# Kernel optimization log

Measured on AMD Instinct MI355X. Metric: run time of the kernel, lower is better.

## Reference

```python
import jax, jax.numpy as jnp
import numpy as np

S, V = 16, 8                 # node embedding irreps: 16x0e + 8x1o
GEO = 3 * V                  # flattened vector feature dims
OUT = 8                      # output irreps: 8x0e
RADIUS = 5.0
NUM_BASIS = 20               # radius * basis_density_per_A
ACT_NORM = 1.6789717         # e3nn normalize2mom constant for silu under N(0,1)
SQ3 = 3.0 ** 0.5
W_MSG = S*S + V*S + S*V + V*V        # 576 = weight_numel of node x sh -> node TP
W_REC = (S*S + V*V) * OUT            # 2560 = weight_numel of node x node -> 8x0e TP


def _mlp(x, w0, w1):
    # e3nn FullyConnectedNet: randn weights, matmul scaled by 1/sqrt(fan_in),
    # hidden activation is second-moment-normalized silu, last layer linear.
    h = jax.nn.silu(x @ (w0 / np.sqrt(w0.shape[0]))) * ACT_NORM
    return h @ (w1 / np.sqrt(w1.shape[0]))


def _sh(vec):
    # o3.spherical_harmonics lmax=1, normalize=True, normalization='component':
    # Y0 = 1, Y1 = sqrt(3) * unit_vector
    r = vec / jnp.linalg.norm(vec, axis=-1, keepdims=True)
    return jnp.ones((vec.shape[0], 1), vec.dtype), SQ3 * r


def _split(f):
    return f[:, :S], f[:, S:].reshape(-1, V, 3)


def _tp_node_sh(xf, y0, y1, w):
    # FullyConnectedTensorProduct (Sx0e+Vx1o) x (1x0e+1x1o) -> (Sx0e+Vx1o), external per-edge weights.
    # CG (e3nn wigner_3j): 0x0->0: 1; 1x1->0: delta/sqrt3; 0x1->1,1x0->1: delta/sqrt3.
    # path_weight = sqrt((2l_out+1)/fan_in), fan_in per output irrep = S*1 + V*1.
    xs, xv = _split(xf)
    o = 0
    wA = w[:, o:o + S*S].reshape(-1, S, S); o += S*S   # 0e x 0e -> 0e
    wB = w[:, o:o + V*S].reshape(-1, V, S); o += V*S   # 1o x 1o -> 0e
    wC = w[:, o:o + S*V].reshape(-1, S, V); o += S*V   # 0e x 1o -> 1o
    wD = w[:, o:].reshape(-1, V, V)                    # 1o x 0e -> 1o
    fan = float(S + V)
    pw0 = (1.0 / fan) ** 0.5
    pw1 = (3.0 / fan) ** 0.5
    out_s = pw0 * (jnp.einsum('eu,euw->ew', xs * y0, wA)
                   + jnp.einsum('eui,ei,euw->ew', xv, y1, wB) / SQ3)
    out_v = (pw1 / SQ3) * (jnp.einsum('eu,ei,euw->ewi', xs, y1, wC)
                           + jnp.einsum('eui,euw->ewi', xv * y0[..., None], wD))
    return jnp.concatenate([out_s, out_v.reshape(-1, GEO)], axis=1)


def _tp_rec(xf, yf, w):
    # FullyConnectedTensorProduct (node) x (node) -> OUTx0e, external per-edge weights.
    xs, xv = _split(xf)
    ys, yv = _split(yf)
    w1 = w[:, :S*S*OUT].reshape(-1, S, S, OUT)
    w2 = w[:, S*S*OUT:].reshape(-1, V, V, OUT)
    pw = (1.0 / float(S*S + V*V)) ** 0.5
    return pw * (jnp.einsum('eu,ev,euvw->ew', xs, ys, w1)
                 + jnp.einsum('eui,evi,euvw->ew', xv, yv, w2) / SQ3)


def _dist_embed(d):
    # soft_one_hot_linspace(basis='smooth_finite', cutoff=True) * sqrt(num_basis)
    values = jnp.linspace(0.0, RADIUS, NUM_BASIS + 2)[1:-1]
    step = RADIUS / (NUM_BASIS + 1)
    diff = (d[:, None] - values) / step
    sus = lambda t: jnp.where(t > 0.0, jnp.exp(-1.0 / jnp.where(t > 0.0, t, 1.0)), 0.0)
    return 1.14136 * np.exp(2.0) * sus(diff + 1.0) * sus(1.0 - diff) * (NUM_BASIS ** 0.5)


def _mp_step(node, pos, src, dst, edge_attr, imp, mw0, mw1, uw0, uw1, is_initial):
    n = node.shape[0]
    vec = pos[dst] - pos[src]
    y0, y1 = _sh(vec)
    tp = _tp_node_sh(node[src], y0, y1, _mlp(edge_attr, mw0, mw1))
    deg = src.shape[0] / n
    msgs = jax.ops.segment_sum(tp, dst, num_segments=n) / (deg ** 0.5)
    msgs = msgs * imp
    scal = _mlp(jnp.concatenate([msgs[:, :S], node[:, :S]], axis=1), uw0, uw1)
    geo = msgs[:, S:] + node[:, S:]
    if not is_initial:
        geo = geo * 0.5
    return jnp.concatenate([scal, geo], axis=1)


def _forward(x, pos, edge_attr, emb_w0, emb_w1, imp0, msg0_w0, msg0_w1, upd0_w0, upd0_w1,
             imp1, msg1_w0, msg1_w1, upd1_w0, upd1_w1, lig_w0, lig_w1, rec_w0, rec_w1,
             edge_index, inter_edge_index):
    src, dst = edge_index[0], edge_index[1]
    node = _mlp(x, emb_w0, emb_w1)                                   # [N, S]
    node = jnp.concatenate([node, jnp.zeros((node.shape[0], GEO), node.dtype)], axis=1)
    node = _mp_step(node, pos, src, dst, edge_attr, imp0, msg0_w0, msg0_w1, upd0_w0, upd0_w1, True)
    node = _mp_step(node, pos, src, dst, edge_attr, imp1, msg1_w0, msg1_w1, upd1_w0, upd1_w1, False)
    rec, lig = inter_edge_index[0], inter_edge_index[1]
    vec = pos[lig] - pos[rec]
    y0, y1 = _sh(vec)
    demb = _dist_embed(jnp.linalg.norm(vec, axis=1))
    lig_emb = _tp_node_sh(node[lig], y0, y1, _mlp(demb, lig_w0, lig_w1))
    return _tp_rec(lig_emb, node[rec], _mlp(demb, rec_w0, rec_w1))    # [E_inter, OUT]


def setup_inputs():
    key = jax.random.key(0)
    ks = iter(jax.random.split(key, 32))
    N, E, EI = 10000, 120000, 40000
    A, B = 10, 5   # len(atom_types), len(bond_types)
    rn = lambda *s: jax.random.normal(next(ks), s, dtype=jnp.float32)
    # edges without self-loops (dst != src) to keep edge_vec nonzero
    src = jax.random.randint(next(ks), (E,), 0, N)
    dst = (src + jax.random.randint(next(ks), (E,), 1, N)) % N
    irec = jax.random.randint(next(ks), (EI,), 0, N)
    ilig = (irec + jax.random.randint(next(ks), (EI,), 1, N)) % N
    return dict(
        x=jax.random.uniform(next(ks), (N, A), dtype=jnp.float32),
        pos=rn(N, 3) * 3.0,
        edge_index=jnp.stack([src, dst]),
        edge_attr=jax.random.uniform(next(ks), (E, B), dtype=jnp.float32),
        inter_edge_index=jnp.stack([irec, ilig]),
        emb_w0=rn(A, 64), emb_w1=rn(64, S),
        imp0=rn(1), msg0_w0=rn(B, 64), msg0_w1=rn(64, W_MSG),
        upd0_w0=rn(2 * S, 64), upd0_w1=rn(64, S),
        imp1=rn(1), msg1_w0=rn(B, 64), msg1_w1=rn(64, W_MSG),
        upd1_w0=rn(2 * S, 64), upd1_w1=rn(64, S),
        lig_w0=rn(NUM_BASIS, 64), lig_w1=rn(64, W_MSG),
        rec_w0=rn(NUM_BASIS, 64), rec_w1=rn(64, W_REC),
    )


def reference(x, pos, edge_index, edge_attr, inter_edge_index,
              emb_w0, emb_w1, imp0, msg0_w0, msg0_w1, upd0_w0, upd0_w1,
              imp1, msg1_w0, msg1_w1, upd1_w0, upd1_w1,
              lig_w0, lig_w1, rec_w0, rec_w1):
    return _forward(x, pos, edge_attr, emb_w0, emb_w1, imp0, msg0_w0, msg0_w1, upd0_w0, upd0_w1,
                    imp1, msg1_w0, msg1_w1, upd1_w0, upd1_w1, lig_w0, lig_w1, rec_w0, rec_w1,
                    edge_index, inter_edge_index)
```

## Files before the change

### kernel.cpp

```cpp
#include <hip/hip_runtime.h>
#include <hip/hip_fp16.h>
#include <cmath>

constexpr float ACT_NORM = 1.6789717f;
constexpr float PW0      = 0.20412414523193154f;
constexpr float PW1      = 0.35355339059327373f;
constexpr float PWREC    = 0.05590169943749474f;
constexpr float INV_SQ3  = 0.57735026918962576f;
constexpr float PW0s     = PW0 * 0.125f;
constexpr float PW1s     = PW1 * 0.125f;
constexpr float PWRECs   = PWREC * 0.125f;

__device__ __forceinline__ float silu_n(float x) {
  return x / (1.f + __expf(-x)) * ACT_NORM;
}

__device__ __forceinline__ unsigned ubcast_lane(unsigned v, int k) {
  return (unsigned)__builtin_amdgcn_readlane((int)v, k);
}

typedef _Float16 h2v __attribute__((ext_vector_type(2)));
typedef _Float16 f16x8 __attribute__((ext_vector_type(8)));
typedef float    f32x4 __attribute__((ext_vector_type(4)));

__device__ __forceinline__ unsigned packh2(float a, float b) {
  h2v p; p.x = (_Float16)a; p.y = (_Float16)b;
  return __builtin_bit_cast(unsigned, p);
}
__device__ __forceinline__ unsigned short f16bits(float a) {
  return __builtin_bit_cast(unsigned short, (_Float16)a);
}
__device__ __forceinline__ float h2f(unsigned short b) {
  return (float)__builtin_bit_cast(_Float16, b);
}
__device__ __forceinline__ float dot2h(unsigned w2, unsigned h2, float acc) {
  return __builtin_amdgcn_fdot2(__builtin_bit_cast(h2v, w2),
                                __builtin_bit_cast(h2v, h2), acc, false);
}
__device__ __forceinline__ float hlo(unsigned d) {
  return (float)__builtin_bit_cast(_Float16, (unsigned short)(d & 0xffffu));
}
__device__ __forceinline__ float hhi(unsigned d) {
  return (float)__builtin_bit_cast(_Float16, (unsigned short)(d >> 16));
}
__device__ __forceinline__ float hsel(unsigned d, int hi) { return hi ? hhi(d) : hlo(d); }
__device__ __forceinline__ unsigned u4sel(const uint4& v, int i) {
  return i == 0 ? v.x : (i == 1 ? v.y : (i == 2 ? v.z : v.w));
}
__device__ __forceinline__ unsigned u2sel(const uint2& v, int i) { return i ? v.y : v.x; }

__device__ __forceinline__ f32x4 mfma16(uint4 a, uint4 b, f32x4 c) {
  return __builtin_amdgcn_mfma_f32_16x16x32_f16(
      __builtin_bit_cast(f16x8, a), __builtin_bit_cast(f16x8, b), c, 0, 0, 0);
}

__global__ __launch_bounds__(256)
void hist_kernel(const int* __restrict__ ei, int* __restrict__ cnt, int E) {
  const int e = blockIdx.x * 256 + threadIdx.x;
  if (e < E) atomicAdd(&cnt[ei[E + e]], 1);
}

__global__ __launch_bounds__(1024)
void scan_kernel(const int* __restrict__ cnt, int* __restrict__ starts, int N) {
  __shared__ int sums[1024];
  const int t = threadIdx.x;
  const int per = (N + 1023) >> 10;
  const int base = t * per;
  int s = 0;
  for (int i = 0; i < per; ++i) {
    const int idx = base + i;
    if (idx < N) s += cnt[idx];
  }
  sums[t] = s;
  __syncthreads();
  for (int off = 1; off < 1024; off <<= 1) {
    int v = (t >= off) ? sums[t - off] : 0;
    __syncthreads();
    sums[t] += v;
    __syncthreads();
  }
  int run = (t > 0) ? sums[t - 1] : 0;
  for (int i = 0; i < per; ++i) {
    const int idx = base + i;
    if (idx < N) { starts[idx] = run; run += cnt[idx]; }
  }
}

__global__ __launch_bounds__(256)
void scatter_kernel(const int* __restrict__ ei, const int* __restrict__ starts,
                    int* __restrict__ cursor, int* __restrict__ eperm, int E) {
  const int e = blockIdx.x * 256 + threadIdx.x;
  if (e < E) {
    const int d = ei[E + e];
    const int r = atomicAdd(&cursor[d], 1);
    eperm[starts[d] + r] = e;
  }
}

__global__ __launch_bounds__(256)
void emb_kernel(const float* __restrict__ x, const float* __restrict__ w0,
                const float* __restrict__ w1, float* __restrict__ node, int N) {
  const int lane = threadIdx.x & 63;
  const int lw   = threadIdx.x >> 6;
  const int gw   = blockIdx.x * 4 + lw;
  __shared__ float sH[4][64];
  const bool valid = gw < N;
  const int n = valid ? gw : 0;
  float acc = 0.f;
#pragma unroll
  for (int a = 0; a < 10; ++a) acc = fmaf(x[n * 10 + a], w0[a * 64 + lane], acc);
  acc *= 0.31622776601683794f;
  sH[lw][lane] = silu_n(acc);
  __syncthreads();
  if (valid) {
    if (lane < 16) {
      float o = 0.f;
#pragma unroll
      for (int k = 0; k < 64; ++k) o = fmaf(sH[lw][k], w1[k * 16 + lane], o);
      node[(size_t)n * 40 + lane] = o * 0.125f;
    } else if (lane < 40) {
      node[(size_t)n * 40 + lane] = 0.f;
    }
  }
}

template <bool HALFMB>
__global__ __launch_bounds__(256)
void upd_kernel(float* __restrict__ node, const void* __restrict__ mbufv,
                const int* __restrict__ starts, const int* __restrict__ cnt,
                const int* __restrict__ eperm,
                const float* __restrict__ w0, const float* __restrict__ w1,
                const float* __restrict__ imp, float geo_scale, float inv_sqrt_deg, int N) {
  const int lane = threadIdx.x & 63;
  const int lw   = threadIdx.x >> 6;
  const int gw   = blockIdx.x * 4 + lw;
  __shared__ float sIn[4][32];
  __shared__ float sH[4][64];
  const bool valid = gw < N;
  const int n = valid ? gw : 0;
  const float mscale = imp[0] * inv_sqrt_deg;

  float m = 0.f;
  if (lane < 40) {
    const int s0 = starts[n], d = cnt[n];
    if (HALFMB) {
      const unsigned short* mb = (const unsigned short*)mbufv;
      for (int j = 0; j < d; ++j)
        m += h2f(mb[(size_t)eperm[s0 + j] * 40 + lane]);
    } else {
      const float* mb = (const float*)mbufv;
      for (int j = 0; j < d; ++j)
        m += mb[(size_t)eperm[s0 + j] * 40 + lane];
    }
  }

  if (lane < 16)      sIn[lw][lane] = m * mscale;
  else if (lane < 32) sIn[lw][lane] = node[(size_t)n * 40 + lane - 16];
  __syncthreads();
  float acc = 0.f;
#pragma unroll
  for (int a = 0; a < 32; ++a) acc = fmaf(sIn[lw][a], w0[a * 64 + lane], acc);
  acc *= 0.17677669529663687f;
  sH[lw][lane] = silu_n(acc);
  __syncthreads();
  if (valid) {
    if (lane < 16) {
      float o = 0.f;
#pragma unroll
      for (int k = 0; k < 64; ++k) o = fmaf(sH[lw][k], w1[k * 16 + lane], o);
      node[(size_t)n * 40 + lane] = o * 0.125f;
    } else if (lane < 40) {
      const size_t gi = (size_t)n * 40 + lane;
      node[gi] = fmaf(m, mscale, node[gi]) * geo_scale;
    }
  }
}

__global__ __launch_bounds__(256)
void inter_h_kernel(const float* __restrict__ pos, const int* __restrict__ iei,
                    const float* __restrict__ lw0, const float* __restrict__ rw0,
                    float* __restrict__ hL, float* __restrict__ hR, int EI) {
  const int lane = threadIdx.x & 63;
  const int lw   = threadIdx.x >> 6;
  const int gw   = blockIdx.x * 4 + lw;
  __shared__ float sD[4][20];
  const bool valid = gw < EI;
  const int e = valid ? gw : 0;
  const int rec = iei[e], lig = iei[EI + e];
  const float dx = pos[lig * 3]     - pos[rec * 3];
  const float dy = pos[lig * 3 + 1] - pos[rec * 3 + 1];
  const float dz = pos[lig * 3 + 2] - pos[rec * 3 + 2];
  const float d = sqrtf(dx * dx + dy * dy + dz * dz);
  if (lane < 20) {
    const float diff = d * 4.2f - (float)(lane + 1);
    const float t1 = diff + 1.f, t2 = 1.f - diff;
    float v = 0.f;
    if (t1 > 0.f && t2 > 0.f) {
      const float C = 1.14136f * 7.3890560989306495f * 4.4721359549995794f;
      v = C * __expf(-1.f / t1 - 1.f / t2);
    }
    sD[lw][lane] = v;
  }
  __syncthreads();
  float a0 = 0.f, a1 = 0.f;
#pragma unroll
  for (int b = 0; b < 20; ++b) {
    const float db = sD[lw][b];
    a0 = fmaf(db, lw0[b * 64 + lane], a0);
    a1 = fmaf(db, rw0[b * 64 + lane], a1);
  }
  a0 *= 0.22360679774997896f;
  a1 *= 0.22360679774997896f;
  if (valid) {
    hL[(size_t)e * 64 + lane] = silu_n(a0);
    hR[(size_t)e * 64 + lane] = silu_n(a1);
  }
}

__global__ __launch_bounds__(256)
void edge_hf_kernel(const float* __restrict__ eattr, const float* __restrict__ w0,
                    uint4* __restrict__ hEf, int E, int nTe) {
  const int gid = blockIdx.x * 256 + threadIdx.x;
  if (gid >= nTe * 128) return;
  const int T = gid >> 7, rem = gid & 127, H = rem >> 6, l = rem & 63;
  int e = T * 16 + (l & 15);
  if (e >= E) e = E - 1;
  const int k0 = H * 32 + (l >> 4) * 8;
  float ea[5];
#pragma unroll
  for (int a = 0; a < 5; ++a) ea[a] = eattr[(size_t)e * 5 + a] * 0.4472135954999579f;
  unsigned q[4];
#pragma unroll
  for (int jj = 0; jj < 4; ++jj) {
    float hh[2];
#pragma unroll
    for (int p = 0; p < 2; ++p) {
      const int k = k0 + jj * 2 + p;
      float acc = 0.f;
#pragma unroll
      for (int a = 0; a < 5; ++a) acc = fmaf(ea[a], w0[a * 64 + k], acc);
      hh[p] = silu_n(acc);
    }
    q[jj] = packh2(hh[0], hh[1]);
  }
  uint4 out; out.x = q[0]; out.y = q[1]; out.z = q[2]; out.w = q[3];
  hEf[gid] = out;
}

template <bool HALFMB>
__global__ __launch_bounds__(256, 2)
void msg_mfma_kernel(const float* __restrict__ node, const float* __restrict__ pos,
                     const int* __restrict__ ei, const float* __restrict__ W1,
                     const uint4* __restrict__ hEf, void* __restrict__ mbufv,
                     int E, int nTe) {
  __shared__ __align__(16) uint4 sB[36 * 128];
  __shared__ __align__(16) unsigned short sFt[4][16][56];
  const int tid = threadIdx.x, lane = tid & 63, wv = tid >> 6;

  for (int j = tid; j < 4608; j += 256) {
    const int t = j >> 7, H = (j >> 6) & 1, l = j & 63;
    const int kb = H * 32 + (l >> 4) * 8;
    const float* src = &W1[(size_t)kb * 576 + t * 16 + (l & 15)];
    uint4 q;
    q.x = packh2(src[0],       src[576]);
    q.y = packh2(src[2 * 576], src[3 * 576]);
    q.z = packh2(src[4 * 576], src[5 * 576]);
    q.w = packh2(src[6 * 576], src[7 * 576]);
    sB[j] = q;
  }
  __syncthreads();

  unsigned short (*fW)[56] = sFt[wv];
  const int er0 = (lane >> 4) * 4;
  const int c   = lane & 15;
  const int cp  = (lane >> 3) & 1;
  const int w   = c & 7;

  for (int T = blockIdx.x * 4 + wv; T < nTe; T += (int)gridDim.x * 4) {
    if (lane < 16) {
      int ge = T * 16 + lane; if (ge >= E) ge = E - 1;
      const int ia = ei[ge], ib = ei[E + ge];
      const float vx = pos[ib * 3]     - pos[ia * 3];
      const float vy = pos[ib * 3 + 1] - pos[ia * 3 + 1];
      const float vz = pos[ib * 3 + 2] - pos[ia * 3 + 2];
      const float rn = rsqrtf(vx * vx + vy * vy + vz * vz);
      fW[lane][40] = f16bits(vx * rn);
      fW[lane][41] = f16bits(vy * rn);
      fW[lane][42] = f16bits(vz * rn);
    }
#pragma unroll
    for (int j = 0; j < 4; ++j) {
      const int e = j * 4 + (lane >> 4);
      int ge = T * 16 + e; if (ge >= E) ge = E - 1;
      const int ns = ei[ge];
      fW[e][c] = f16bits(node[(size_t)ns * 40 + c]);
    }
#pragma unroll
    for (int j = 0; j < 6; ++j) {
      const int flat = j * 64 + lane;
      const int e = flat / 24, q = flat - e * 24;
      const int u = q / 3, i = q - u * 3;
      int ge = T * 16 + e; if (ge >= E) ge = E - 1;
      const int ns = ei[ge];
      fW[e][16 + i * 8 + (u & 1) * 4 + (u >> 1)] = f16bits(node[(size_t)ns * 40 + 16 + q]);
    }
#pragma unroll
    for (int j = 0; j < 2; ++j) {
      const int flat = j * 64 + lane;
      const int e = flat >> 3, u = flat & 7;
      float d = 0.f;
#pragma unroll
      for (int i = 0; i < 3; ++i)
        d = fmaf(h2f(fW[e][16 + i * 8 + (u & 1) * 4 + (u >> 1)]), h2f(fW[e][40 + i]), d);
      fW[e][48 + u] = f16bits(d);
    }

    const uint4 a0 = hEf[T * 128 + lane];
    const uint4 a1 = hEf[T * 128 + 64 + lane];

    uint4 xsR[4][2], dpR[4];
    uint2 xvR[4][3];
    float rf[4][3];
#pragma unroll
    for (int r = 0; r < 4; ++r) {
      const int e = er0 + r;
      xsR[r][0] = *(const uint4*)&fW[e][0];
      xsR[r][1] = *(const uint4*)&fW[e][8];
      dpR[r]    = *(const uint4*)&fW[e][48];
#pragma unroll
      for (int i = 0; i < 3; ++i) {
        xvR[r][i] = *(const uint2*)&fW[e][16 + i * 8 + cp * 4];
        rf[r][i]  = h2f(fW[e][40 + i]);
      }
    }

    float o_s[4] = {0.f, 0.f, 0.f, 0.f};
    float sxw[4] = {0.f, 0.f, 0.f, 0.f};
    float ov[3][4];
#pragma unroll
    for (int i = 0; i < 3; ++i)
#pragma unroll
      for (int r = 0; r < 4; ++r) ov[i][r] = 0.f;

    uint4 b0 = sB[lane], b1 = sB[64 + lane];
#pragma unroll
    for (int t = 0; t < 36; ++t) {
      uint4 n0, n1;
      if (t < 35) { n0 = sB[(t + 1) * 128 + lane]; n1 = sB[(t + 1) * 128 + 64 + lane]; }
      f32x4 C = {0.f, 0.f, 0.f, 0.f};
      C = mfma16(a0, b0, C);
      C = mfma16(a1, b1, C);
      if (t < 16) {
#pragma unroll
        for (int r = 0; r < 4; ++r)
          o_s[r] = fmaf(hsel(u4sel(xsR[r][t >> 3], (t >> 1) & 3), t & 1), C[r], o_s[r]);
      } else if (t < 24) {
        const int u = t - 16;
#pragma unroll
        for (int r = 0; r < 4; ++r)
          o_s[r] = fmaf(hsel(u4sel(dpR[r], u >> 1), u & 1), C[r], o_s[r]);
      } else if (t < 32) {
        const int j = t - 24;
#pragma unroll
        for (int r = 0; r < 4; ++r) {
          const int idx = 2 * j + cp;
          sxw[r] = fmaf(hsel(u4sel(xsR[r][idx >> 3], (idx >> 1) & 3), idx & 1), C[r], sxw[r]);
        }
      } else {
        const int j = t - 32;
#pragma unroll
        for (int i = 0; i < 3; ++i)
#pragma unroll
          for (int r = 0; r < 4; ++r)
            ov[i][r] = fmaf(hsel(u2sel(xvR[r][i], j >> 1), j & 1), C[r], ov[i][r]);
      }
      if (t < 35) { b0 = n0; b1 = n1; }
    }

#pragma unroll
    for (int r = 0; r < 4; ++r) {
      const int ge = T * 16 + er0 + r;
      const bool valid = ge < E;
      const float sv = PW0s * o_s[r];
      float vv[3];
#pragma unroll
      for (int i = 0; i < 3; ++i) {
        float v = fmaf(PW1s * rf[r][i], sxw[r], PW0s * ov[i][r]);
        v += __shfl_xor(v, 8);
        vv[i] = v;
      }
      if (valid) {
        if (HALFMB) {
          unsigned short* mb = (unsigned short*)mbufv + (size_t)ge * 40;
          mb[c] = f16bits(sv);
          if ((lane & 8) == 0) {
#pragma unroll
            for (int i = 0; i < 3; ++i) mb[16 + w * 3 + i] = f16bits(vv[i]);
          }
        } else {
          float* mb = (float*)mbufv + (size_t)ge * 40;
          mb[c] = sv;
          if ((lane & 8) == 0) {
#pragma unroll
            for (int i = 0; i < 3; ++i) mb[16 + w * 3 + i] = vv[i];
          }
        }
      }
    }
  }
}

template <int MODE>
__global__ __launch_bounds__(512, 2)
void tp_kernel(const float* __restrict__ node, const float* __restrict__ pos,
               const int* __restrict__ ei, const float* __restrict__ eattr,
               const float* __restrict__ w0, const float* __restrict__ W1,
               const float* __restrict__ hSrc, float* __restrict__ out, int E) {
  __shared__ __align__(16) uint4 sWa[32 * 64];
  __shared__ __align__(16) uint4 sWb[32 * 64];
  __shared__ unsigned sWc[32 * 64];
  __shared__ float sF[8][6][27];
  const int tid  = threadIdx.x;
  const int lane = tid & 63;
  const int wv   = tid >> 6;

  for (int j = tid; j < 2048; j += 512) {
    const int kp = j >> 6, l = j & 63;
    const float* s0 = &W1[(2 * kp) * 576 + l];
    const float* s1 = s0 + 576;
    uint4 qa, qb;
    qa.x = packh2(s0[0],   s1[0]);
    qa.y = packh2(s0[64],  s1[64]);
    qa.z = packh2(s0[128], s1[128]);
    qa.w = packh2(s0[192], s1[192]);
    qb.x = packh2(s0[256], s1[256]);
    qb.y = packh2(s0[320], s1[320]);
    qb.z = packh2(s0[384], s1[384]);
    qb.w = packh2(s0[448], s1[448]);
    sWa[j] = qa;
    sWb[j] = qb;
    sWc[j] = packh2(s0[512], s1[512]);
  }
  __syncthreads();

  float w0r[5];
  if (MODE == 0) {
#pragma unroll
    for (int a = 0; a < 5; ++a) w0r[a] = w0[a * 64 + lane] * 0.4472135954999579f;
  }
  const int kl2 = (lane & 31) * 2;

  const int nB = (E + 47) / 48;
  for (int b = blockIdx.x; b < nB; b += (int)gridDim.x) {
    const int ebase = b * 48 + wv * 6;
    int outn[6], nsrc[6];
    bool val[6];
    unsigned hp[6];
#pragma unroll
    for (int s = 0; s < 6; ++s) {
      const int e0 = ebase + s;
      val[s] = e0 < E;
      const int e = val[s] ? e0 : 0;
      const int ia = ei[e], ib = ei[E + e];
      if (MODE == 0) { nsrc[s] = ia; outn[s] = ib; }
      else           { nsrc[s] = ib; outn[s] = e;  }
      const float vx = pos[ib * 3]     - pos[ia * 3];
      const float vy = pos[ib * 3 + 1] - pos[ia * 3 + 1];
      const float vz = pos[ib * 3 + 2] - pos[ia * 3 + 2];
      const float rn = rsqrtf(vx * vx + vy * vy + vz * vz);
      const float rx = vx * rn, ry = vy * rn, rz = vz * rn;
      float h;
      if (MODE == 0) {
        float acc = 0.f;
#pragma unroll
        for (int a = 0; a < 5; ++a) acc = fmaf(eattr[(size_t)e * 5 + a], w0r[a], acc);
        h = silu_n(acc);
      } else {
        h = hSrc[(size_t)e * 64 + lane];
      }
      hp[s] = packh2(__shfl(h, kl2), __shfl(h, kl2 + 1));
      if (lane < 16) {
        sF[wv][s][lane] = node[(size_t)nsrc[s] * 40 + lane];
      } else if (lane < 24) {
        const int u = lane - 16;
        const float x0 = node[(size_t)nsrc[s] * 40 + 16 + u * 3];
        const float x1 = node[(size_t)nsrc[s] * 40 + 16 + u * 3 + 1];
        const float x2 = node[(size_t)nsrc[s] * 40 + 16 + u * 3 + 2];
        sF[wv][s][16 + u] = x0 * rx + x1 * ry + x2 * rz;
      } else if (lane < 27) {
        sF[wv][s][24 + (lane - 24)] = (lane == 24) ? rx : ((lane == 25) ? ry : rz);
      }
    }

    float wacc[6][9];
#pragma unroll
    for (int s = 0; s < 6; ++s)
#pragma unroll
      for (int t = 0; t < 9; ++t) wacc[s][t] = 0.f;

    uint4 qa0 = sWa[lane], qb0 = sWb[lane];
    unsigned qc0 = sWc[lane];
#pragma unroll 4
    for (int kp = 0; kp < 32; ++kp) {
      const int kn = (kp + 1) & 31;
      const uint4 qa1 = sWa[kn * 64 + lane];
      const uint4 qb1 = sWb[kn * 64 + lane];
      const unsigned qc1 = sWc[kn * 64 + lane];
#pragma unroll
      for (int s = 0; s < 6; ++s) {
        const unsigned hv2 = ubcast_lane(hp[s], kp);
        wacc[s][0] = dot2h(qa0.x, hv2, wacc[s][0]);
        wacc[s][1] = dot2h(qa0.y, hv2, wacc[s][1]);
        wacc[s][2] = dot2h(qa0.z, hv2, wacc[s][2]);
        wacc[s][3] = dot2h(qa0.w, hv2, wacc[s][3]);
        wacc[s][4] = dot2h(qb0.x, hv2, wacc[s][4]);
        wacc[s][5] = dot2h(qb0.y, hv2, wacc[s][5]);
        wacc[s][6] = dot2h(qb0.z, hv2, wacc[s][6]);
        wacc[s][7] = dot2h(qb0.w, hv2, wacc[s][7]);
        wacc[s][8] = dot2h(qc0,   hv2, wacc[s][8]);
      }
      qa0 = qa1; qb0 = qb1; qc0 = qc1;
    }

    const int ub  = lane >> 4;
    const int ub2 = lane >> 3;
#pragma unroll
    for (int s = 0; s < 6; ++s) {
      float cs = 0.f;
#pragma unroll
      for (int t = 0; t < 6; ++t)
        cs = fmaf(PW0s * sF[wv][s][ub + 4 * t], wacc[s][t], cs);
      cs += __shfl_xor(cs, 16);
      cs += __shfl_xor(cs, 32);

      const float rx = sF[wv][s][24], ry = sF[wv][s][25], rz = sF[wv][s][26];
      const float* xp = &node[(size_t)nsrc[s] * 40 + 16 + ub2 * 3];
      const float xv0 = xp[0], xv1 = xp[1], xv2 = xp[2];
      const float sxw = PW1s * (sF[wv][s][ub2] * wacc[s][6] + sF[wv][s][ub2 + 8] * wacc[s][7]);
      float cv0 = fmaf(PW0s * xv0, wacc[s][8], sxw * rx);
      float cv1 = fmaf(PW0s * xv1, wacc[s][8], sxw * ry);
      float cv2 = fmaf(PW0s * xv2, wacc[s][8], sxw * rz);
      cv0 += __shfl_xor(cv0, 8); cv0 += __shfl_xor(cv0, 16); cv0 += __shfl_xor(cv0, 32);
      cv1 += __shfl_xor(cv1, 8); cv1 += __shfl_xor(cv1, 16); cv1 += __shfl_xor(cv1, 32);
      cv2 += __shfl_xor(cv2, 8); cv2 += __shfl_xor(cv2, 16); cv2 += __shfl_xor(cv2, 32);

      if (val[s]) {
        const size_t ob = (size_t)outn[s] * 40;
        if (lane < 16) out[ob + lane] = cs;
        if (lane < 8) {
          out[ob + 16 + lane * 3]     = cv0;
          out[ob + 16 + lane * 3 + 1] = cv1;
          out[ob + 16 + lane * 3 + 2] = cv2;
        }
      }
    }
  }
}

__global__ __launch_bounds__(512)
void pack_h_kernel(const float* __restrict__ h, uint4* __restrict__ hPf, int nT) {
  const int gid = blockIdx.x * 512 + threadIdx.x;
  if (gid >= nT * 128) return;
  const int l = gid & 63;
  const int H = (gid >> 6) & 1;
  const int T = gid >> 7;
  const int e = T * 16 + (l & 15);
  const int kb = H * 32 + (l >> 4) * 8;
  const float* src = &h[(size_t)e * 64 + kb];
  uint4 q;
  q.x = packh2(src[0], src[1]);
  q.y = packh2(src[2], src[3]);
  q.z = packh2(src[4], src[5]);
  q.w = packh2(src[6], src[7]);
  hPf[gid] = q;
}

__global__ __launch_bounds__(256)
void pack_d_kernel(const float* __restrict__ ligE, const float* __restrict__ node,
                   const int* __restrict__ iei, unsigned short* __restrict__ Dt, int EI) {
  const int gid = blockIdx.x * 256 + threadIdx.x;
  if (gid >= EI * 64) return;
  const int e = gid >> 6, rem = gid & 63;
  const int b = rem >> 5, u = (rem >> 2) & 7, vi = rem & 3;
  const int v = 2 * vi + b;
  const int rec = iei[e];
  const float* xp = &ligE[(size_t)e * 40 + 16 + u * 3];
  const float* yp = &node[(size_t)rec * 40 + 16 + v * 3];
  const float d = (xp[0] * yp[0] + xp[1] * yp[1] + xp[2] * yp[2]) * INV_SQ3;
  Dt[gid] = f16bits(d);
}

__global__ __launch_bounds__(512, 2)
void rec_kernel(const float* __restrict__ node, const float* __restrict__ ligE,
                const int* __restrict__ iei, const float* __restrict__ RW1,
                const uint4* __restrict__ hPf, const uint2* __restrict__ Dt2,
                float* __restrict__ out, int nT) {
  __shared__ __align__(16) uint4 sB[4096];
  __shared__ __align__(16) unsigned short sFeat[8][320];
  const int tid = threadIdx.x, lane = tid & 63, wv = tid >> 6;
  const int cg = blockIdx.y;

  for (int j = tid; j < 4096; j += 512) {
    const int t = j >> 7, H = (j >> 6) & 1, l = j & 63;
    const int kb = H * 32 + (l >> 4) * 8;
    const float* src = &RW1[(size_t)kb * 2560 + cg * 512 + t * 16 + (l & 15)];
    uint4 q;
    q.x = packh2(src[0],        src[2560]);
    q.y = packh2(src[2 * 2560], src[3 * 2560]);
    q.z = packh2(src[4 * 2560], src[5 * 2560]);
    q.w = packh2(src[6 * 2560], src[7 * 2560]);
    sB[j] = q;
  }
  __syncthreads();

  unsigned short* fW = sFeat[wv];
  const int er0 = (lane >> 4) * 4;
  const int bpar = (lane >> 3) & 1;
  const int c    = lane & 7;
  const int se = lane >> 2, si = lane & 3;

  for (int T = blockIdx.x * 8 + wv; T < nT; T += (int)gridDim.x * 8) {
    const uint4 a0 = hPf[(T * 2 + 0) * 64 + lane];
    const uint4 a1 = hPf[(T * 2 + 1) * 64 + lane];
    const int eg = T * 16 + se;

    if (cg < 4) {
      const int rn = iei[eg];
      const float4 yv = *(const float4*)&node[(size_t)rn * 40 + si * 4];
      *(unsigned*)&fW[(se * 2 + 0) * 8 + 2 * si] = packh2(yv.x, yv.z);
      *(unsigned*)&fW[(se * 2 + 1) * 8 + 2 * si] = packh2(yv.y, yv.w);
      fW[256 + se * 4 + si] = f16bits(ligE[(size_t)eg * 40 + cg * 4 + si]);
    }

    float o[4] = {0.f, 0.f, 0.f, 0.f};
    uint4 b0 = sB[lane], b1 = sB[64 + lane];

    if (cg < 4) {
      uint2 xsR[4]; uint4 ysR[4];
#pragma unroll
      for (int r = 0; r < 4; ++r) {
        const int er = er0 + r;
        ysR[r] = *(const uint4*)&fW[(er * 2 + bpar) * 8];
        xsR[r] = *(const uint2*)&fW[256 + er * 4];
      }
#pragma unroll
      for (int t = 0; t < 32; ++t) {
        uint4 n0, n1;
        if (t < 31) { n0 = sB[(t + 1) * 128 + lane]; n1 = sB[(t + 1) * 128 + 64 + lane]; }
        f32x4 C = {0.f, 0.f, 0.f, 0.f};
        C = mfma16(a0, b0, C);
        C = mfma16(a1, b1, C);
        const int up = t >> 3, vi = t & 7;
#pragma unroll
        for (int r = 0; r < 4; ++r) {
          const float xs = hsel(u2sel(xsR[r], up >> 1), up & 1);
          const float ys = hsel(u4sel(ysR[r], vi >> 1), vi & 1);
          o[r] = fmaf(xs * ys, C[r], o[r]);
        }
        if (t < 31) { b0 = n0; b1 = n1; }
      }
    } else {
#pragma unroll
      for (int pass = 0; pass < 2; ++pass) {
        uint2 dR[4][4];
#pragma unroll
        for (int r = 0; r < 4; ++r) {
          const int e = T * 16 + er0 + r;
#pragma unroll
          for (int uu = 0; uu < 4; ++uu)
            dR[r][uu] = Dt2[(size_t)e * 16 + bpar * 8 + pass * 4 + uu];
        }
#pragma unroll
        for (int tt = 0; tt < 16; ++tt) {
          const int t = pass * 16 + tt;
          uint4 n0, n1;
          if (t < 31) { n0 = sB[(t + 1) * 128 + lane]; n1 = sB[(t + 1) * 128 + 64 + lane]; }
          f32x4 C = {0.f, 0.f, 0.f, 0.f};
          C = mfma16(a0, b0, C);
          C = mfma16(a1, b1, C);
          const int uu = tt >> 2, vi = tt & 3;
#pragma unroll
          for (int r = 0; r < 4; ++r) {
            const float f = hsel(u2sel(dR[r][uu], vi >> 1), vi & 1);
            o[r] = fmaf(f, C[r], o[r]);
          }
          if (t < 31) { b0 = n0; b1 = n1; }
        }
      }
    }

#pragma unroll
    for (int r = 0; r < 4; ++r) {
      const float v = o[r] + __shfl_xor(o[r], 8);
      if ((lane & 8) == 0)
        atomicAdd(&out[(size_t)(T * 16 + er0 + r) * 8 + c], v * PWRECs);
    }
  }
}

extern "C" void kernel_launch(void* const* d_in, const int* in_sizes, int n_in,
                              void* d_out, int out_size, void* d_ws, size_t ws_size,
                              hipStream_t stream) {
  (void)n_in;
  const float* x      = (const float*)d_in[0];
  const float* pos    = (const float*)d_in[1];
  const int*   ei     = (const int*)  d_in[2];
  const float* eattr  = (const float*)d_in[3];
  const int*   iei    = (const int*)  d_in[4];
  const float* emb_w0 = (const float*)d_in[5];
  const float* emb_w1 = (const float*)d_in[6];
  const float* imp0   = (const float*)d_in[7];
  const float* m0w0   = (const float*)d_in[8];
  const float* m0w1   = (const float*)d_in[9];
  const float* u0w0   = (const float*)d_in[10];
  const float* u0w1   = (const float*)d_in[11];
  const float* imp1   = (const float*)d_in[12];
  const float* m1w0   = (const float*)d_in[13];
  const float* m1w1   = (const float*)d_in[14];
  const float* u1w0   = (const float*)d_in[15];
  const float* u1w1   = (const float*)d_in[16];
  const float* lw0    = (const float*)d_in[17];
  const float* lw1    = (const float*)d_in[18];
  const float* rw0    = (const float*)d_in[19];
  const float* rw1    = (const float*)d_in[20];

  const int N  = in_sizes[1] / 3;
  const int E  = in_sizes[2] / 2;
  const int EI = in_sizes[4] / 2;

  float* node = (float*)d_ws;
  float* hL   = node + (size_t)N * 40;
  float* hR   = hL + (size_t)EI * 64;
  float* ligE = hR + (size_t)EI * 64;
  float* outp = (float*)d_out;

  uint4* hEf   = (uint4*)hL;
  float* mbase = hL + (size_t)E * 32;
  const size_t csrInts = (size_t)3 * N + E + 16;
  const size_t need32  = ((size_t)N * 40 + (size_t)E * 32 + (size_t)E * 40 + csrInts) * 4;
  const bool   halfmb  = need32 > ws_size;
  const size_t mbFl    = halfmb ? ((size_t)E * 20) : ((size_t)E * 40);
  void* mbuf   = (void*)mbase;
  int*  cnt    = (int*)(mbase + mbFl);
  int*  starts = cnt + N;
  int*  cursor = starts + N;
  int*  eperm  = cursor + N;

  uint4*          hPf = (uint4*)hL;
  unsigned short* Dt  = (unsigned short*)hR;

  const float inv_sqrt_deg = 1.0f / sqrtf((float)E / (float)N);
  const int nodeBlocks  = (N + 3) / 4;
  const int interBlocks = (EI + 3) / 4;
  const int nT  = EI / 16;
  const int nTe = (E + 15) / 16;
  const int hfBlocks = (nTe * 128 + 255) / 256;
  const int eBlocks  = (E + 255) / 256;

  hipMemsetAsync(cnt, 0, (size_t)N * sizeof(int), stream);
  hipMemsetAsync(cursor, 0, (size_t)N * sizeof(int), stream);
  hist_kernel<<<eBlocks, 256, 0, stream>>>(ei, cnt, E);
  scan_kernel<<<1, 1024, 0, stream>>>(cnt, starts, N);
  scatter_kernel<<<eBlocks, 256, 0, stream>>>(ei, starts, cursor, eperm, E);

  emb_kernel<<<nodeBlocks, 256, 0, stream>>>(x, emb_w0, emb_w1, node, N);

  edge_hf_kernel<<<hfBlocks, 256, 0, stream>>>(eattr, m0w0, hEf, E, nTe);
  if (halfmb) {
    msg_mfma_kernel<true><<<512, 256, 0, stream>>>(node, pos, ei, m0w1, hEf, mbuf, E, nTe);
    upd_kernel<true><<<nodeBlocks, 256, 0, stream>>>(node, mbuf, starts, cnt, eperm,
                                                     u0w0, u0w1, imp0, 1.0f, inv_sqrt_deg, N);
  } else {
    msg_mfma_kernel<false><<<512, 256, 0, stream>>>(node, pos, ei, m0w1, hEf, mbuf, E, nTe);
    upd_kernel<false><<<nodeBlocks, 256, 0, stream>>>(node, mbuf, starts, cnt, eperm,
                                                      u0w0, u0w1, imp0, 1.0f, inv_sqrt_deg, N);
  }

  edge_hf_kernel<<<hfBlocks, 256, 0, stream>>>(eattr, m1w0, hEf, E, nTe);
  if (halfmb) {
    msg_mfma_kernel<true><<<512, 256, 0, stream>>>(node, pos, ei, m1w1, hEf, mbuf, E, nTe);
    upd_kernel<true><<<nodeBlocks, 256, 0, stream>>>(node, mbuf, starts, cnt, eperm,
                                                     u1w0, u1w1, imp1, 0.5f, inv_sqrt_deg, N);
  } else {
    msg_mfma_kernel<false><<<512, 256, 0, stream>>>(node, pos, ei, m1w1, hEf, mbuf, E, nTe);
    upd_kernel<false><<<nodeBlocks, 256, 0, stream>>>(node, mbuf, starts, cnt, eperm,
                                                      u1w0, u1w1, imp1, 0.5f, inv_sqrt_deg, N);
  }

  inter_h_kernel<<<interBlocks, 256, 0, stream>>>(pos, iei, lw0, rw0, hL, hR, EI);
  tp_kernel<1><<<512, 512, 0, stream>>>(node, pos, iei, nullptr, nullptr, lw1, hL, ligE, EI);

  pack_h_kernel<<<(nT * 128 + 511) / 512, 512, 0, stream>>>(hR, hPf, nT);
  pack_d_kernel<<<(EI * 64 + 255) / 256, 256, 0, stream>>>(ligE, node, iei, Dt, EI);

  hipMemsetAsync(outp, 0, (size_t)out_size * sizeof(float), stream);
  rec_kernel<<<dim3(102, 5), 512, 0, stream>>>(node, ligE, iei, rw1, hPf, (const uint2*)Dt,
                                               outp, nT);
}
```

Baseline: 387.4 us.

## Fuse edge hidden MLP into message kernel and prepack B weights once

Removes the separate edge_hf kernel and computes the edge-attribute hidden layer (silu of eattr·w0) inside the MFMA message kernel in LDS, avoiding the global write and read of the packed hidden buffer. The fp16 packing of W1 moves to a small pack_b kernel so blocks copy prepacked tiles instead of repacking per block. The last four B tiles are held in registers to shrink LDS. The workspace layout is rearranged and the half-precision message-buffer fallback is dropped, so there is no longer a check against ws_size. This costs more registers and per-tile redundant work in the message kernel.

```diff
diff --git a/kernel.cpp b/kernel.cpp
--- a/kernel.cpp
+++ b/kernel.cpp
@@ -98,6 +98,21 @@
 }
 
 __global__ __launch_bounds__(256)
+void pack_b_kernel(const float* __restrict__ W1, uint4* __restrict__ Bp) {
+  const int gid = blockIdx.x * 256 + threadIdx.x;
+  if (gid >= 36 * 128) return;
+  const int t = gid >> 7, H = (gid >> 6) & 1, l = gid & 63;
+  const int kb = H * 32 + (l >> 4) * 8;
+  const float* src = &W1[(size_t)kb * 576 + t * 16 + (l & 15)];
+  uint4 q;
+  q.x = packh2(src[0],       src[576]);
+  q.y = packh2(src[2 * 576], src[3 * 576]);
+  q.z = packh2(src[4 * 576], src[5 * 576]);
+  q.w = packh2(src[6 * 576], src[7 * 576]);
+  Bp[gid] = q;
+}
+
+__global__ __launch_bounds__(256)
 void emb_kernel(const float* __restrict__ x, const float* __restrict__ w0,
                 const float* __restrict__ w1, float* __restrict__ node, int N) {
   const int lane = threadIdx.x & 63;
@@ -124,9 +139,8 @@
   }
 }
 
-template <bool HALFMB>
 __global__ __launch_bounds__(256)
-void upd_kernel(float* __restrict__ node, const void* __restrict__ mbufv,
+void upd_kernel(float* __restrict__ node, const float* __restrict__ mbuf,
                 const int* __restrict__ starts, const int* __restrict__ cnt,
                 const int* __restrict__ eperm,
                 const float* __restrict__ w0, const float* __restrict__ w1,
@@ -143,15 +157,8 @@
   float m = 0.f;
   if (lane < 40) {
     const int s0 = starts[n], d = cnt[n];
-    if (HALFMB) {
-      const unsigned short* mb = (const unsigned short*)mbufv;
-      for (int j = 0; j < d; ++j)
-        m += h2f(mb[(size_t)eperm[s0 + j] * 40 + lane]);
-    } else {
-      const float* mb = (const float*)mbufv;
-      for (int j = 0; j < d; ++j)
-        m += mb[(size_t)eperm[s0 + j] * 40 + lane];
-    }
+    for (int j = 0; j < d; ++j)
+      m += mbuf[(size_t)eperm[s0 + j] * 40 + lane];
   }
 
   if (lane < 16)      sIn[lw][lane] = m * mscale;
@@ -217,66 +224,54 @@
   }
 }
 
-__global__ __launch_bounds__(256)
-void edge_hf_kernel(const float* __restrict__ eattr, const float* __restrict__ w0,
-                    uint4* __restrict__ hEf, int E, int nTe) {
-  const int gid = blockIdx.x * 256 + threadIdx.x;
-  if (gid >= nTe * 128) return;
-  const int T = gid >> 7, rem = gid & 127, H = rem >> 6, l = rem & 63;
-  int e = T * 16 + (l & 15);
-  if (e >= E) e = E - 1;
-  const int k0 = H * 32 + (l >> 4) * 8;
-  float ea[5];
-#pragma unroll
-  for (int a = 0; a < 5; ++a) ea[a] = eattr[(size_t)e * 5 + a] * 0.4472135954999579f;
-  unsigned q[4];
-#pragma unroll
-  for (int jj = 0; jj < 4; ++jj) {
-    float hh[2];
-#pragma unroll
-    for (int p = 0; p < 2; ++p) {
-      const int k = k0 + jj * 2 + p;
-      float acc = 0.f;
-#pragma unroll
-      for (int a = 0; a < 5; ++a) acc = fmaf(ea[a], w0[a * 64 + k], acc);
-      hh[p] = silu_n(acc);
-    }
-    q[jj] = packh2(hh[0], hh[1]);
-  }
-  uint4 out; out.x = q[0]; out.y = q[1]; out.z = q[2]; out.w = q[3];
-  hEf[gid] = out;
-}
-
-template <bool HALFMB>
 __global__ __launch_bounds__(256, 2)
 void msg_mfma_kernel(const float* __restrict__ node, const float* __restrict__ pos,
-                     const int* __restrict__ ei, const float* __restrict__ W1,
-                     const uint4* __restrict__ hEf, void* __restrict__ mbufv,
-                     int E, int nTe) {
-  __shared__ __align__(16) uint4 sB[36 * 128];
-  __shared__ __align__(16) unsigned short sFt[4][16][56];
+                     const int* __restrict__ ei, const float* __restrict__ eattr,
+                     const float* __restrict__ w0, const uint4* __restrict__ Bp,
+                     float* __restrict__ mbuf, int E, int nTe) {
+  __shared__ __align__(16) uint4 sB[32 * 128];
+  __shared__ __align__(16) unsigned short sFt[4][16][64];
   const int tid = threadIdx.x, lane = tid & 63, wv = tid >> 6;
 
-  for (int j = tid; j < 4608; j += 256) {
-    const int t = j >> 7, H = (j >> 6) & 1, l = j & 63;
-    const int kb = H * 32 + (l >> 4) * 8;
-    const float* src = &W1[(size_t)kb * 576 + t * 16 + (l & 15)];
-    uint4 q;
-    q.x = packh2(src[0],       src[576]);
-    q.y = packh2(src[2 * 576], src[3 * 576]);
-    q.z = packh2(src[4 * 576], src[5 * 576]);
-    q.w = packh2(src[6 * 576], src[7 * 576]);
-    sB[j] = q;
-  }
+  for (int j = tid; j < 4096; j += 256) sB[j] = Bp[j];
   __syncthreads();
 
-  unsigned short (*fW)[56] = sFt[wv];
+  uint4 g32[8];
+#pragma unroll
+  for (int j = 0; j < 8; ++j) g32[j] = Bp[(64 + j) * 64 + lane];
+
+  float w0c[5];
+#pragma unroll
+  for (int a = 0; a < 5; ++a) w0c[a] = w0[a * 64 + lane] * 0.4472135954999579f;
+
+  unsigned short (*fW)[64] = sFt[wv];
   const int er0 = (lane >> 4) * 4;
   const int c   = lane & 15;
   const int cp  = (lane >> 3) & 1;
   const int w   = c & 7;
+  const int el  = lane & 15;
+  const int kb0 = (lane >> 4) * 8;
 
   for (int T = blockIdx.x * 4 + wv; T < nTe; T += (int)gridDim.x * 4) {
+#pragma unroll
+    for (int j = 0; j < 2; ++j) {
+      const int flat = j * 64 + lane;
+      if (flat < 80) {
+        const int e = flat / 5, a = flat - e * 5;
+        int ge = T * 16 + e; if (ge >= E) ge = E - 1;
+        fW[e][56 + a] = f16bits(eattr[(size_t)ge * 5 + a]);
+      }
+    }
+#pragma unroll
+    for (int e = 0; e < 16; ++e) {
+      float acc = 0.f;
+#pragma unroll
+      for (int a = 0; a < 5; ++a) acc = fmaf(h2f(fW[e][56 + a]), w0c[a], acc);
+      fW[e][lane] = f16bits(silu_n(acc));
+    }
+    const uint4 a0 = *(const uint4*)&fW[el][kb0];
+    const uint4 a1 = *(const uint4*)&fW[el][32 + kb0];
+
     if (lane < 16) {
       int ge = T * 16 + lane; if (ge >= E) ge = E - 1;
       const int ia = ei[ge], ib = ei[E + ge];
@@ -315,9 +310,6 @@
       fW[e][48 + u] = f16bits(d);
     }
 
-    const uint4 a0 = hEf[T * 128 + lane];
-    const uint4 a1 = hEf[T * 128 + 64 + lane];
-
     uint4 xsR[4][2], dpR[4];
     uint2 xvR[4][3];
     float rf[4][3];
@@ -344,9 +336,9 @@
 
     uint4 b0 = sB[lane], b1 = sB[64 + lane];
 #pragma unroll
-    for (int t = 0; t < 36; ++t) {
+    for (int t = 0; t < 32; ++t) {
       uint4 n0, n1;
-      if (t < 35) { n0 = sB[(t + 1) * 128 + lane]; n1 = sB[(t + 1) * 128 + 64 + lane]; }
+      if (t < 31) { n0 = sB[(t + 1) * 128 + lane]; n1 = sB[(t + 1) * 128 + 64 + lane]; }
       f32x4 C = {0.f, 0.f, 0.f, 0.f};
       C = mfma16(a0, b0, C);
       C = mfma16(a1, b1, C);
@@ -359,22 +351,26 @@
 #pragma unroll
         for (int r = 0; r < 4; ++r)
           o_s[r] = fmaf(hsel(u4sel(dpR[r], u >> 1), u & 1), C[r], o_s[r]);
-      } else if (t < 32) {
+      } else {
         const int j = t - 24;
 #pragma unroll
         for (int r = 0; r < 4; ++r) {
           const int idx = 2 * j + cp;
           sxw[r] = fmaf(hsel(u4sel(xsR[r][idx >> 3], (idx >> 1) & 3), idx & 1), C[r], sxw[r]);
         }
-      } else {
-        const int j = t - 32;
-#pragma unroll
-        for (int i = 0; i < 3; ++i)
-#pragma unroll
-          for (int r = 0; r < 4; ++r)
-            ov[i][r] = fmaf(hsel(u2sel(xvR[r][i], j >> 1), j & 1), C[r], ov[i][r]);
-      }
-      if (t < 35) { b0 = n0; b1 = n1; }
+      }
+      if (t < 31) { b0 = n0; b1 = n1; }
+    }
+#pragma unroll
+    for (int j = 0; j < 4; ++j) {
+      f32x4 C = {0.f, 0.f, 0.f, 0.f};
+      C = mfma16(a0, g32[j * 2], C);
+      C = mfma16(a1, g32[j * 2 + 1], C);
+#pragma unroll
+      for (int i = 0; i < 3; ++i)
+#pragma unroll
+        for (int r = 0; r < 4; ++r)
+          ov[i][r] = fmaf(hsel(u2sel(xvR[r][i], j >> 1), j & 1), C[r], ov[i][r]);
     }
 
 #pragma unroll
@@ -390,20 +386,11 @@
         vv[i] = v;
       }
       if (valid) {
-        if (HALFMB) {
-          unsigned short* mb = (unsigned short*)mbufv + (size_t)ge * 40;
-          mb[c] = f16bits(sv);
-          if ((lane & 8) == 0) {
-#pragma unroll
-            for (int i = 0; i < 3; ++i) mb[16 + w * 3 + i] = f16bits(vv[i]);
-          }
-        } else {
-          float* mb = (float*)mbufv + (size_t)ge * 40;
-          mb[c] = sv;
-          if ((lane & 8) == 0) {
-#pragma unroll
-            for (int i = 0; i < 3; ++i) mb[16 + w * 3 + i] = vv[i];
-          }
+        float* mb = mbuf + (size_t)ge * 40;
+        mb[c] = sv;
+        if ((lane & 8) == 0) {
+#pragma unroll
+          for (int i = 0; i < 3; ++i) mb[16 + w * 3 + i] = vv[i];
         }
       }
     }
@@ -701,7 +688,7 @@
 extern "C" void kernel_launch(void* const* d_in, const int* in_sizes, int n_in,
                               void* d_out, int out_size, void* d_ws, size_t ws_size,
                               hipStream_t stream) {
-  (void)n_in;
+  (void)n_in; (void)ws_size;
   const float* x      = (const float*)d_in[0];
   const float* pos    = (const float*)d_in[1];
   const int*   ei     = (const int*)  d_in[2];
@@ -729,23 +716,20 @@
   const int EI = in_sizes[4] / 2;
 
   float* node = (float*)d_ws;
-  float* hL   = node + (size_t)N * 40;
+  float* regA = node + (size_t)N * 40;
+  float* outp = (float*)d_out;
+
+  int*   cnt    = (int*)regA;
+  int*   starts = cnt + N;
+  int*   cursor = starts + N;
+  int*   eperm  = cursor + N;
+  float* bbase  = (float*)(eperm + E);
+  uint4* Bp     = (uint4*)bbase;
+  float* mbuf   = bbase + 36 * 128 * 4;
+
+  float* hL   = regA;
   float* hR   = hL + (size_t)EI * 64;
   float* ligE = hR + (size_t)EI * 64;
-  float* outp = (float*)d_out;
-
-  uint4* hEf   = (uint4*)hL;
-  float* mbase = hL + (size_t)E * 32;
-  const size_t csrInts = (size_t)3 * N + E + 16;
-  const size_t need32  = ((size_t)N * 40 + (size_t)E * 32 + (size_t)E * 40 + csrInts) * 4;
-  const bool   halfmb  = need32 > ws_size;
-  const size_t mbFl    = halfmb ? ((size_t)E * 20) : ((size_t)E * 40);
-  void* mbuf   = (void*)mbase;
-  int*  cnt    = (int*)(mbase + mbFl);
-  int*  starts = cnt + N;
-  int*  cursor = starts + N;
-  int*  eperm  = cursor + N;
-
   uint4*          hPf = (uint4*)hL;
   unsigned short* Dt  = (unsigned short*)hR;
 
@@ -754,8 +738,7 @@
   const int interBlocks = (EI + 3) / 4;
   const int nT  = EI / 16;
   const int nTe = (E + 15) / 16;
-  const int hfBlocks = (nTe * 128 + 255) / 256;
-  const int eBlocks  = (E + 255) / 256;
+  const int eBlocks = (E + 255) / 256;
 
   hipMemsetAsync(cnt, 0, (size_t)N * sizeof(int), stream);
   hipMemsetAsync(cursor, 0, (size_t)N * sizeof(int), stream);
@@ -765,27 +748,15 @@
 
   emb_kernel<<<nodeBlocks, 256, 0, stream>>>(x, emb_w0, emb_w1, node, N);
 
-  edge_hf_kernel<<<hfBlocks, 256, 0, stream>>>(eattr, m0w0, hEf, E, nTe);
-  if (halfmb) {
-    msg_mfma_kernel<true><<<512, 256, 0, stream>>>(node, pos, ei, m0w1, hEf, mbuf, E, nTe);
-    upd_kernel<true><<<nodeBlocks, 256, 0, stream>>>(node, mbuf, starts, cnt, eperm,
-                                                     u0w0, u0w1, imp0, 1.0f, inv_sqrt_deg, N);
-  } else {
-    msg_mfma_kernel<false><<<512, 256, 0, stream>>>(node, pos, ei, m0w1, hEf, mbuf, E, nTe);
-    upd_kernel<false><<<nodeBlocks, 256, 0, stream>>>(node, mbuf, starts, cnt, eperm,
-                                                      u0w0, u0w1, imp0, 1.0f, inv_sqrt_deg, N);
-  }
-
-  edge_hf_kernel<<<hfBlocks, 256, 0, stream>>>(eattr, m1w0, hEf, E, nTe);
-  if (halfmb) {
-    msg_mfma_kernel<true><<<512, 256, 0, stream>>>(node, pos, ei, m1w1, hEf, mbuf, E, nTe);
-    upd_kernel<true><<<nodeBlocks, 256, 0, stream>>>(node, mbuf, starts, cnt, eperm,
-                                                     u1w0, u1w1, imp1, 0.5f, inv_sqrt_deg, N);
-  } else {
-    msg_mfma_kernel<false><<<512, 256, 0, stream>>>(node, pos, ei, m1w1, hEf, mbuf, E, nTe);
-    upd_kernel<false><<<nodeBlocks, 256, 0, stream>>>(node, mbuf, starts, cnt, eperm,
-                                                      u1w0, u1w1, imp1, 0.5f, inv_sqrt_deg, N);
-  }
+  pack_b_kernel<<<18, 256, 0, stream>>>(m0w1, Bp);
+  msg_mfma_kernel<<<512, 256, 0, stream>>>(node, pos, ei, eattr, m0w0, Bp, mbuf, E, nTe);
+  upd_kernel<<<nodeBlocks, 256, 0, stream>>>(node, mbuf, starts, cnt, eperm,
+                                             u0w0, u0w1, imp0, 1.0f, inv_sqrt_deg, N);
+
+  pack_b_kernel<<<18, 256, 0, stream>>>(m1w1, Bp);
+  msg_mfma_kernel<<<512, 256, 0, stream>>>(node, pos, ei, eattr, m1w0, Bp, mbuf, E, nTe);
+  upd_kernel<<<nodeBlocks, 256, 0, stream>>>(node, mbuf, starts, cnt, eperm,
+                                             u1w0, u1w1, imp1, 0.5f, inv_sqrt_deg, N);
 
   inter_h_kernel<<<interBlocks, 256, 0, stream>>>(pos, iei, lw0, rw0, hL, hR, EI);
   tp_kernel<1><<<512, 512, 0, stream>>>(node, pos, iei, nullptr, nullptr, lw1, hL, ligE, EI);
```

New measurement: 381.7 us. Within noise of the previous version (-1.5%).
